# Kernel optimization log

Measured on AMD Instinct MI355X. Metric: run time of the kernel, lower is better.

Reference implementation:

```python
import jax, jax.numpy as jnp
import numpy as np

NUM_NODES = 200000   # graph size
E = 128              # embedding_size
B = 256              # batch of target nodes
M = 8                # num_metapaths
L = 64               # walk length (number of (n1,n2,e) triples per metapath)
NUM_EDGE_TYPE = 8
H = 8                # num_heads (hardcoded in module)


def setup_inputs() -> dict:
    key = jax.random.key(0)
    ks = jax.random.split(key, 10)
    # walks: last dim = (n1, n2, edge_type)
    n12 = jax.random.randint(ks[0], (B, M, L, 2), 0, NUM_NODES)
    ety = jax.random.randint(ks[1], (B, M, L, 1), 0, NUM_EDGE_TYPE)
    node_mp_walks = jnp.concatenate([n12, ety], axis=-1)
    node_idx = jax.random.randint(ks[2], (B,), 0, NUM_NODES)
    mp_type_idx = jnp.arange(M)
    # fc1(onehot(n)) == node_table[n] + fc1_b  (node_table = fc1.weight.T)
    node_table = jax.random.normal(ks[3], (NUM_NODES, E), dtype=jnp.float32) * 0.1
    fc1_b = jnp.zeros((E,), dtype=jnp.float32)
    edge_table = jax.random.normal(ks[4], (NUM_EDGE_TYPE, E), dtype=jnp.float32) * 0.1
    # Indexed_LinearFC_List: one (E,E) linear per metapath
    W_mp = jax.random.normal(ks[5], (M, E, E), dtype=jnp.float32) * 0.05
    b_mp = jnp.zeros((M, E), dtype=jnp.float32)
    # MultiheadAttention params (embed_dim=E, num_heads=H, eval mode -> no dropout)
    Wqkv = jax.random.normal(ks[6], (3 * E, E), dtype=jnp.float32) * 0.05
    bqkv = jnp.zeros((3 * E,), dtype=jnp.float32)
    Wo = jax.random.normal(ks[7], (E, E), dtype=jnp.float32) * 0.05
    bo = jnp.zeros((E,), dtype=jnp.float32)
    return dict(node_idx=node_idx, mp_type_idx=mp_type_idx, node_mp_walks=node_mp_walks,
                node_table=node_table, fc1_b=fc1_b, edge_table=edge_table,
                W_mp=W_mp, b_mp=b_mp, Wqkv=Wqkv, bqkv=bqkv, Wo=Wo, bo=bo)


def reference(node_idx, mp_type_idx, node_mp_walks, node_table, fc1_b, edge_table,
              W_mp, b_mp, Wqkv, bqkv, Wo, bo):
    n1 = node_mp_walks[..., 0]          # [B,M,L]
    n2 = node_mp_walks[..., 1]
    e = node_mp_walks[..., 2]
    # gather node/edge embeddings (fc1 over one-hot == table row + bias)
    n1_vec = node_table[n1] + fc1_b     # [B,M,L,E]
    n2_vec = node_table[n2] + fc1_b     # [B,M,L,E]
    edge_vec = edge_table[e]            # [B,M,L,E]
    # elementwise fuse + mean over walk steps
    mp_agg_0 = jnp.mean(n1_vec * n2_vec * edge_vec, axis=2)        # [B,M,E]
    # per-metapath indexed linear
    Wsel = W_mp[mp_type_idx]            # [M,E,E]
    bsel = b_mp[mp_type_idx]            # [M,E]
    mp_agg_1 = jnp.einsum('bme,meo->bmo', mp_agg_0, Wsel) + bsel   # [B,M,E]
    # self-attention over metapaths (torch MHA, seq-first layout: [M,B,E])
    x = jnp.transpose(mp_agg_1, (1, 0, 2))                         # [M,B,E]
    qkv = x @ Wqkv.T + bqkv                                        # [M,B,3E]
    q, k, v = jnp.split(qkv, 3, axis=-1)
    hd = E // H
    q = q.reshape(M, B, H, hd)
    k = k.reshape(M, B, H, hd)
    v = v.reshape(M, B, H, hd)
    scores = jnp.einsum('mbhd,nbhd->bhmn', q, k) / jnp.sqrt(jnp.float32(hd))
    attn = jax.nn.softmax(scores, axis=-1)                         # [B,H,M,M]
    o = jnp.einsum('bhmn,nbhd->mbhd', attn, v).reshape(M, B, E)
    attn_output = o @ Wo.T + bo                                    # [M,B,E]
    return attn_output
```

## Files before the change

kernel.cpp:

```cpp
#include <hip/hip_runtime.h>

#define B 256
#define M 8
#define L 64
#define E 128
#define H 8
#define HD 16
#define NET 8
#define E3 384

__global__ __launch_bounds__(256) void k_transpose(
    const float* __restrict__ Wqkv, const float* __restrict__ Wo,
    float* __restrict__ WqkvT, float* __restrict__ WoT) {
  int idx = blockIdx.x * 256 + threadIdx.x;
  if (idx < E * E3) {
    int e = idx / E3;
    int o = idx - e * E3;
    WqkvT[idx] = Wqkv[o * E + e];
  } else {
    int j = idx - E * E3;
    int e = j >> 7, o = j & 127;
    WoT[j] = Wo[o * E + e];
  }
}

__global__ __launch_bounds__(256) void k_fused(
    const int* __restrict__ walks, const float* __restrict__ node_table,
    const float* __restrict__ fc1_b, const float* __restrict__ edge_table,
    const int* __restrict__ mp_type_idx,
    const float* __restrict__ W_mp, const float* __restrict__ b_mp,
    const float* __restrict__ WqkvT, const float* __restrict__ bqkv,
    const float* __restrict__ WoT, const float* __restrict__ bo,
    float* __restrict__ out) {
  __shared__ int   s_idx[M][L][3];
  __shared__ float s_et[NET * E];
  __shared__ float s_x[M][E];
  __shared__ float s_y[M][E];
  __shared__ float s_qkv[M][E3 + 1];
  __shared__ float s_sc[H][M][M];
  __shared__ float s_o[M][E];
  __shared__ int   s_mp[M];

  int b = blockIdx.x;
  int t = threadIdx.x;
  int g = t >> 5, lane = t & 31;

  const int* wb = walks + b * (M * L * 3);
  #pragma unroll
  for (int i = 0; i < 6; ++i) ((int*)s_idx)[i * 256 + t] = wb[i * 256 + t];
  #pragma unroll
  for (int i = 0; i < 4; ++i) s_et[i * 256 + t] = edge_table[i * 256 + t];
  if (t < M) s_mp[t] = mp_type_idx[t];
  __syncthreads();

  const float4* nt4 = (const float4*)node_table;
  float4 fb = ((const float4*)fc1_b)[lane];
  {
    float4 acc = make_float4(0.f, 0.f, 0.f, 0.f);
    for (int l0 = 0; l0 < L; l0 += 8) {
      float4 a[8], c[8];
      #pragma unroll
      for (int i = 0; i < 8; ++i) {
        int n1 = s_idx[g][l0 + i][0];
        int n2 = s_idx[g][l0 + i][1];
        a[i] = nt4[n1 * 32 + lane];
        c[i] = nt4[n2 * 32 + lane];
      }
      #pragma unroll
      for (int i = 0; i < 8; ++i) {
        int et = s_idx[g][l0 + i][2];
        float4 ev = ((const float4*)(s_et + et * E))[lane];
        acc.x += (a[i].x + fb.x) * (c[i].x + fb.x) * ev.x;
        acc.y += (a[i].y + fb.y) * (c[i].y + fb.y) * ev.y;
        acc.z += (a[i].z + fb.z) * (c[i].z + fb.z) * ev.z;
        acc.w += (a[i].w + fb.w) * (c[i].w + fb.w) * ev.w;
      }
    }
    const float inv = 1.0f / (float)L;
    acc.x *= inv; acc.y *= inv; acc.z *= inv; acc.w *= inv;
    ((float4*)s_x[g])[lane] = acc;
  }
  __syncthreads();

  {
    int mp = s_mp[g];
    const float4* W4 = (const float4*)(W_mp + mp * E * E);
    float4 acc = make_float4(0.f, 0.f, 0.f, 0.f);
    for (int e = 0; e < E; ++e) {
      float x = s_x[g][e];
      float4 w = W4[e * 32 + lane];
      acc.x += x * w.x; acc.y += x * w.y; acc.z += x * w.z; acc.w += x * w.w;
    }
    float4 bb = ((const float4*)(b_mp + mp * E))[lane];
    acc.x += bb.x; acc.y += bb.y; acc.z += bb.z; acc.w += bb.w;
    ((float4*)s_y[g])[lane] = acc;
  }
  __syncthreads();

  #pragma unroll
  for (int p = 0; p < 3; ++p) {
    float4 acc = make_float4(0.f, 0.f, 0.f, 0.f);
    for (int e = 0; e < E; ++e) {
      float x = s_y[g][e];
      float4 w = ((const float4*)(WqkvT + e * E3))[p * 32 + lane];
      acc.x += x * w.x; acc.y += x * w.y; acc.z += x * w.z; acc.w += x * w.w;
    }
    float4 bb = ((const float4*)bqkv)[p * 32 + lane];
    int base = p * 128 + lane * 4;
    s_qkv[g][base + 0] = acc.x + bb.x;
    s_qkv[g][base + 1] = acc.y + bb.y;
    s_qkv[g][base + 2] = acc.z + bb.z;
    s_qkv[g][base + 3] = acc.w + bb.w;
  }
  __syncthreads();

  #pragma unroll
  for (int i = 0; i < 2; ++i) {
    int idx = i * 256 + t;
    int h = idx >> 6;
    int mq = (idx >> 3) & 7;
    int n = idx & 7;
    float s = 0.f;
    #pragma unroll
    for (int d = 0; d < HD; ++d)
      s += s_qkv[mq][h * HD + d] * s_qkv[n][E + h * HD + d];
    s_sc[h][mq][n] = s * 0.25f;
  }
  __syncthreads();

  if (t < 64) {
    int h = t >> 3, mq = t & 7;
    float mx = -1e30f;
    #pragma unroll
    for (int n = 0; n < 8; ++n) mx = fmaxf(mx, s_sc[h][mq][n]);
    float ex[8];
    float sum = 0.f;
    #pragma unroll
    for (int n = 0; n < 8; ++n) { ex[n] = __expf(s_sc[h][mq][n] - mx); sum += ex[n]; }
    float inv = 1.0f / sum;
    #pragma unroll
    for (int n = 0; n < 8; ++n) s_sc[h][mq][n] = ex[n] * inv;
  }
  __syncthreads();

  #pragma unroll
  for (int i = 0; i < 4; ++i) {
    int idx = i * 256 + t;
    int mq = idx >> 7;
    int col = idx & 127;
    int h = col >> 4;
    float s = 0.f;
    #pragma unroll
    for (int n = 0; n < 8; ++n)
      s += s_sc[h][mq][n] * s_qkv[n][2 * E + col];
    s_o[mq][col] = s;
  }
  __syncthreads();

  {
    const float4* Wo4 = (const float4*)WoT;
    float4 acc = make_float4(0.f, 0.f, 0.f, 0.f);
    for (int e = 0; e < E; ++e) {
      float x = s_o[g][e];
      float4 w = Wo4[e * 32 + lane];
      acc.x += x * w.x; acc.y += x * w.y; acc.z += x * w.z; acc.w += x * w.w;
    }
    float4 bb = ((const float4*)bo)[lane];
    acc.x += bb.x; acc.y += bb.y; acc.z += bb.z; acc.w += bb.w;
    ((float4*)(out + (g * B + b) * E))[lane] = acc;
  }
}

extern "C" void kernel_launch(void* const* d_in, const int* in_sizes, int n_in,
                              void* d_out, int out_size, void* d_ws, size_t ws_size,
                              hipStream_t stream) {
  const int*   mp_type_idx = (const int*)d_in[1];
  const int*   walks       = (const int*)d_in[2];
  const float* node_table  = (const float*)d_in[3];
  const float* fc1_b       = (const float*)d_in[4];
  const float* edge_table  = (const float*)d_in[5];
  const float* W_mp        = (const float*)d_in[6];
  const float* b_mp        = (const float*)d_in[7];
  const float* Wqkv        = (const float*)d_in[8];
  const float* bqkv        = (const float*)d_in[9];
  const float* Wo          = (const float*)d_in[10];
  const float* bo          = (const float*)d_in[11];
  float* out = (float*)d_out;

  char* ws = (char*)d_ws;
  float* WqkvT = (float*)(ws);
  float* WoT   = (float*)(ws + (256 << 10));

  k_transpose<<<dim3(256), dim3(256), 0, stream>>>(Wqkv, Wo, WqkvT, WoT);
  k_fused<<<dim3(B), dim3(256), 0, stream>>>(
      walks, node_table, fc1_b, edge_table, mp_type_idx,
      W_mp, b_mp, WqkvT, bqkv, WoT, bo, out);
}
```

Baseline: 203.7 us.

## Quadruple block threads to 1024 and split walk gathers and GEMVs across them

The fused kernel moves from 256 to 1024 threads per block. The walk-step gather is split four ways per metapath and combined with a shared-memory reduction. The matrix-vector stages are remapped to one output column per thread, with each weight load reused across several metapath rows. The aim is more memory-level parallelism for the random node-table gathers and for the weight reads, since only 256 blocks are launched. In exchange it adds an extra barrier and reduction, leaves some threads idle in later stages, and switches to scalar rather than float4 weight loads.

```diff
diff --git a/kernel.cpp b/kernel.cpp
--- a/kernel.cpp
+++ b/kernel.cpp
@@ -24,7 +24,7 @@
   }
 }
 
-__global__ __launch_bounds__(256) void k_fused(
+__global__ __launch_bounds__(1024) void k_fused(
     const int* __restrict__ walks, const float* __restrict__ node_table,
     const float* __restrict__ fc1_b, const float* __restrict__ edge_table,
     const int* __restrict__ mp_type_idx,
@@ -32,43 +32,45 @@
     const float* __restrict__ WqkvT, const float* __restrict__ bqkv,
     const float* __restrict__ WoT, const float* __restrict__ bo,
     float* __restrict__ out) {
-  __shared__ int   s_idx[M][L][3];
-  __shared__ float s_et[NET * E];
-  __shared__ float s_x[M][E];
-  __shared__ float s_y[M][E];
-  __shared__ float s_qkv[M][E3 + 1];
-  __shared__ float s_sc[H][M][M];
-  __shared__ float s_o[M][E];
-  __shared__ int   s_mp[M];
+  __shared__ int    s_idx[M][L][3];
+  __shared__ float  s_et[NET * E];
+  __shared__ float4 s_red[32][32];
+  __shared__ float  s_x[M][E];
+  __shared__ float  s_y[M][E];
+  __shared__ float  s_qkv[M][E3 + 1];
+  __shared__ float  s_sc[H][M][M];
+  __shared__ float  s_o[M][E];
+  __shared__ int    s_mp[M];
 
   int b = blockIdx.x;
   int t = threadIdx.x;
   int g = t >> 5, lane = t & 31;
 
   const int* wb = walks + b * (M * L * 3);
-  #pragma unroll
-  for (int i = 0; i < 6; ++i) ((int*)s_idx)[i * 256 + t] = wb[i * 256 + t];
-  #pragma unroll
-  for (int i = 0; i < 4; ++i) s_et[i * 256 + t] = edge_table[i * 256 + t];
+  for (int idx = t; idx < M * L * 3; idx += 1024) ((int*)s_idx)[idx] = wb[idx];
+  s_et[t] = edge_table[t];
   if (t < M) s_mp[t] = mp_type_idx[t];
   __syncthreads();
 
-  const float4* nt4 = (const float4*)node_table;
-  float4 fb = ((const float4*)fc1_b)[lane];
   {
+    const float4* nt4 = (const float4*)node_table;
+    float4 fb = ((const float4*)fc1_b)[lane];
+    int m = g >> 2, q = g & 3;
     float4 acc = make_float4(0.f, 0.f, 0.f, 0.f);
-    for (int l0 = 0; l0 < L; l0 += 8) {
+    #pragma unroll
+    for (int bi = 0; bi < 2; ++bi) {
+      int l0 = q * 16 + bi * 8;
       float4 a[8], c[8];
       #pragma unroll
       for (int i = 0; i < 8; ++i) {
-        int n1 = s_idx[g][l0 + i][0];
-        int n2 = s_idx[g][l0 + i][1];
+        int n1 = s_idx[m][l0 + i][0];
+        int n2 = s_idx[m][l0 + i][1];
         a[i] = nt4[n1 * 32 + lane];
         c[i] = nt4[n2 * 32 + lane];
       }
       #pragma unroll
       for (int i = 0; i < 8; ++i) {
-        int et = s_idx[g][l0 + i][2];
+        int et = s_idx[m][l0 + i][2];
         float4 ev = ((const float4*)(s_et + et * E))[lane];
         acc.x += (a[i].x + fb.x) * (c[i].x + fb.x) * ev.x;
         acc.y += (a[i].y + fb.y) * (c[i].y + fb.y) * ev.y;
@@ -76,50 +78,51 @@
         acc.w += (a[i].w + fb.w) * (c[i].w + fb.w) * ev.w;
       }
     }
+    s_red[g][lane] = acc;
+  }
+  __syncthreads();
+  if (t < 256) {
+    int m = t >> 5, ln = t & 31;
+    float4 s = s_red[m * 4][ln];
+    #pragma unroll
+    for (int q = 1; q < 4; ++q) {
+      float4 v = s_red[m * 4 + q][ln];
+      s.x += v.x; s.y += v.y; s.z += v.z; s.w += v.w;
+    }
     const float inv = 1.0f / (float)L;
-    acc.x *= inv; acc.y *= inv; acc.z *= inv; acc.w *= inv;
-    ((float4*)s_x[g])[lane] = acc;
+    s.x *= inv; s.y *= inv; s.z *= inv; s.w *= inv;
+    ((float4*)s_x[m])[ln] = s;
   }
   __syncthreads();
 
   {
-    int mp = s_mp[g];
-    const float4* W4 = (const float4*)(W_mp + mp * E * E);
-    float4 acc = make_float4(0.f, 0.f, 0.f, 0.f);
-    for (int e = 0; e < E; ++e) {
-      float x = s_x[g][e];
-      float4 w = W4[e * 32 + lane];
-      acc.x += x * w.x; acc.y += x * w.y; acc.z += x * w.z; acc.w += x * w.w;
-    }
-    float4 bb = ((const float4*)(b_mp + mp * E))[lane];
-    acc.x += bb.x; acc.y += bb.y; acc.z += bb.z; acc.w += bb.w;
-    ((float4*)s_y[g])[lane] = acc;
+    int m = t >> 7, o = t & 127;
+    int mp = s_mp[m];
+    const float* W = W_mp + mp * E * E;
+    float acc = 0.f;
+    for (int e = 0; e < E; ++e)
+      acc += s_x[m][e] * W[e * E + o];
+    s_y[m][o] = acc + b_mp[mp * E + o];
   }
   __syncthreads();
 
-  #pragma unroll
-  for (int p = 0; p < 3; ++p) {
-    float4 acc = make_float4(0.f, 0.f, 0.f, 0.f);
+  if (t < 768) {
+    int half = t / 384;
+    int o = t - half * 384;
+    float acc[4] = {0.f, 0.f, 0.f, 0.f};
     for (int e = 0; e < E; ++e) {
-      float x = s_y[g][e];
-      float4 w = ((const float4*)(WqkvT + e * E3))[p * 32 + lane];
-      acc.x += x * w.x; acc.y += x * w.y; acc.z += x * w.z; acc.w += x * w.w;
+      float w = WqkvT[e * E3 + o];
+      #pragma unroll
+      for (int j = 0; j < 4; ++j) acc[j] += s_y[half * 4 + j][e] * w;
     }
-    float4 bb = ((const float4*)bqkv)[p * 32 + lane];
-    int base = p * 128 + lane * 4;
-    s_qkv[g][base + 0] = acc.x + bb.x;
-    s_qkv[g][base + 1] = acc.y + bb.y;
-    s_qkv[g][base + 2] = acc.z + bb.z;
-    s_qkv[g][base + 3] = acc.w + bb.w;
+    float bias = bqkv[o];
+    #pragma unroll
+    for (int j = 0; j < 4; ++j) s_qkv[half * 4 + j][o] = acc[j] + bias;
   }
   __syncthreads();
 
-  #pragma unroll
-  for (int i = 0; i < 2; ++i) {
-    int idx = i * 256 + t;
-    int h = idx >> 6;
-    int mq = (idx >> 3) & 7;
-    int n = idx & 7;
+  if (t < 512) {
+    int h = t >> 6, mq = (t >> 3) & 7, n = t & 7;
     float s = 0.f;
     #pragma unroll
     for (int d = 0; d < HD; ++d)
@@ -143,12 +146,8 @@
   }
   __syncthreads();
 
-  #pragma unroll
-  for (int i = 0; i < 4; ++i) {
-    int idx = i * 256 + t;
-    int mq = idx >> 7;
-    int col = idx & 127;
-    int h = col >> 4;
+  {
+    int mq = t >> 7, col = t & 127, h = col >> 4;
     float s = 0.f;
     #pragma unroll
     for (int n = 0; n < 8; ++n)
@@ -157,17 +156,17 @@
   }
   __syncthreads();
 
-  {
-    const float4* Wo4 = (const float4*)WoT;
-    float4 acc = make_float4(0.f, 0.f, 0.f, 0.f);
+  if (t < 512) {
+    int pm = t >> 7, o = t & 127;
+    float acc[2] = {0.f, 0.f};
     for (int e = 0; e < E; ++e) {
-      float x = s_o[g][e];
-      float4 w = Wo4[e * 32 + lane];
-      acc.x += x * w.x; acc.y += x * w.y; acc.z += x * w.z; acc.w += x * w.w;
+      float w = WoT[e * E + o];
+      acc[0] += s_o[pm * 2][e] * w;
+      acc[1] += s_o[pm * 2 + 1][e] * w;
     }
-    float4 bb = ((const float4*)bo)[lane];
-    acc.x += bb.x; acc.y += bb.y; acc.z += bb.z; acc.w += bb.w;
-    ((float4*)(out + (g * B + b) * E))[lane] = acc;
+    float bias = bo[o];
+    out[((pm * 2) * B + b) * E + o]     = acc[0] + bias;
+    out[((pm * 2 + 1) * B + b) * E + o] = acc[1] + bias;
   }
 }
 
@@ -192,7 +191,7 @@
   float* WoT   = (float*)(ws + (256 << 10));
 
   k_transpose<<<dim3(256), dim3(256), 0, stream>>>(Wqkv, Wo, WqkvT, WoT);
-  k_fused<<<dim3(B), dim3(256), 0, stream>>>(
+  k_fused<<<dim3(B), dim3(1024), 0, stream>>>(
       walks, node_table, fc1_b, edge_table, mp_type_idx,
       W_mp, b_mp, WqkvT, bqkv, WoT, bo, out);
 }
```

Measured after the change: 189.7 us (median of 2 runs). -6.9%, faster.
